# Performance work log

Hardware: AMD Instinct MI355X
Metric: run time of the kernel (lower is better)

The kernel has to match this reference:

```python
import jax, jax.numpy as jnp
import numpy as np

B, S, D, H = 2, 2048, 1024, 16
DH = D // H


def setup_inputs() -> dict:
    key = jax.random.key(0)
    ks = jax.random.split(key, 6)
    scale = 0.02
    X = jax.random.normal(ks[0], (B, S, D), dtype=jnp.float32)
    masks = jax.random.randint(ks[1], (B, S), 0, 2).astype(jnp.int32)
    Wq = jax.random.normal(ks[2], (D, D), dtype=jnp.float32) * scale
    Wk = jax.random.normal(ks[3], (D, D), dtype=jnp.float32) * scale
    Wv = jax.random.normal(ks[4], (D, D), dtype=jnp.float32) * scale
    Wo = jax.random.normal(ks[5], (D, D), dtype=jnp.float32) * scale
    return {"X": X, "masks": masks, "Wq": Wq, "Wk": Wk, "Wv": Wv, "Wo": Wo}


def reference(X, masks, Wq, Wk, Wv, Wo):
    b, s, d = X.shape
    masks_b = masks.astype(bool)                       # [B,S] key validity
    lookahead = jnp.triu(jnp.ones((s, s), dtype=bool), 1)  # [S,S] future positions
    pad = ~masks_b[:, None, :]                         # [B,1,S] -> invalid keys
    invalid = pad | lookahead[None, :, :]              # [B,S,S]
    valid = (~invalid)[:, None, :, :].astype(X.dtype)  # [B,1,S,S]

    def split_heads(Y):  # [B,S,D] -> [B,H,S,DH]
        return Y.reshape(b, s, H, DH).transpose(0, 2, 1, 3)

    Q = split_heads(X @ Wq.T)
    K = split_heads(X @ Wk.T)
    V = split_heads(X @ Wv.T)

    Qn = Q / jnp.sqrt(jnp.sum(Q * Q, axis=-1, keepdims=True))
    Kn = K / jnp.sqrt(jnp.sum(K * K, axis=-1, keepdims=True))

    scores = jnp.einsum('bhqd,bhkd->bhqk', Qn, Kn)     # cosine similarities
    att = jax.nn.relu(scores) * valid                  # relu + causal/pad mask
    ctx = jnp.einsum('bhqk,bhkd->bhqd', att, V)
    ctx = ctx * masks_b[:, None, :, None].astype(X.dtype)  # zero padded queries

    out = ctx.transpose(0, 2, 1, 3).reshape(b, s, d)
    return out @ Wo.T
```

## Files before the change

### kernel.cpp

```cpp
#include <hip/hip_runtime.h>
#include <hip/hip_bf16.h>

#define BB 2
#define SS 2048
#define DD 1024
#define HH 16
#define MMR (BB*SS)
#define ND3 3072

typedef __hip_bfloat16 bf;
typedef __bf16 bf16x8 __attribute__((ext_vector_type(8)));
typedef float f32x4 __attribute__((ext_vector_type(4)));
typedef float f32x16 __attribute__((ext_vector_type(16)));

#define VMCNT(n) asm volatile("s_waitcnt vmcnt(" #n ")" ::: "memory")

__device__ __forceinline__ f32x4 mfma16(bf16x8 a, bf16x8 b, f32x4 c) {
    return __builtin_amdgcn_mfma_f32_16x16x32_bf16(a, b, c, 0, 0, 0);
}
__device__ __forceinline__ f32x16 mfma32(bf16x8 a, bf16x8 b, f32x16 c) {
    return __builtin_amdgcn_mfma_f32_32x32x16_bf16(a, b, c, 0, 0, 0);
}
__device__ __forceinline__ unsigned cvt_pk_bf16(float lo, float hi) {
    unsigned r;
    asm("v_cvt_pk_bf16_f32 %0, %1, %2" : "=v"(r) : "v"(lo), "v"(hi));
    return r;
}
__device__ __forceinline__ void pl32swap(unsigned& a, unsigned& b) {
    asm("v_permlane32_swap_b32 %0, %1" : "+v"(a), "+v"(b));
}
__device__ __forceinline__ void glds16(const bf* g, bf* l) {
    __builtin_amdgcn_global_load_lds(
        (const __attribute__((address_space(1))) void*)g,
        (__attribute__((address_space(3))) void*)l,
        16, 0, 0);
}

__global__ __launch_bounds__(256) void k_convert(const float* __restrict__ X,
                                                 const float* __restrict__ Wq,
                                                 const float* __restrict__ Wk,
                                                 const float* __restrict__ Wv,
                                                 const float* __restrict__ Wo,
                                                 bf* __restrict__ Xb,
                                                 bf* __restrict__ Wqkv,
                                                 bf* __restrict__ Wob) {
    const int bid = blockIdx.x;
    const float* src;
    bf* dst;
    int off;
    if (bid < 4096) {
        src = X; dst = Xb; off = bid;
    } else {
        const int r = (bid - 4096) >> 10;
        src = (r == 0) ? Wq : (r == 1) ? Wk : (r == 2) ? Wv : Wo;
        dst = (r < 3) ? (Wqkv + (size_t)r * 1048576) : Wob;
        off = (bid - 4096) & 1023;
    }
    const int j = (off * 256 + threadIdx.x) * 4;
    float4 v = *(const float4*)(src + j);
    bf tmp[4];
    tmp[0] = __float2bfloat16(v.x);
    tmp[1] = __float2bfloat16(v.y);
    tmp[2] = __float2bfloat16(v.z);
    tmp[3] = __float2bfloat16(v.w);
    *(uint2*)(dst + j) = *(const uint2*)tmp;
}

__global__ __launch_bounds__(512, 6) void k_gemm8(const bf* __restrict__ A,
                                                  const bf* __restrict__ Bt,
                                                  const int* __restrict__ masks,
                                                  bf* __restrict__ Qn,
                                                  bf* __restrict__ Kn,
                                                  bf* __restrict__ Vt,
                                                  int nx) {
    constexpr int K = 1024;
    constexpr int T = K >> 5;
    __shared__ __align__(16) bf Asm[3][128 * 32];
    __shared__ __align__(16) bf Bsm[3][128 * 32];
    const int tid = threadIdx.x;
    const int w = tid >> 6, lane = tid & 63, g = lane >> 4, rl = lane & 15;
    const int cpx = gridDim.x >> 3;
    const int swz = (blockIdx.x & 7) * cpx + (blockIdx.x >> 3);
    const int m0 = (swz / nx) * 128, n0 = (swz % nx) * 128;
    const int wr = (w >> 1) * 32, wc = (w & 1) * 64;
    const int lrow = lane >> 2, lseg = lane & 3;
    const int xseg = lseg ^ ((lrow >> 1) & 3);

    f32x4 acc[2][4] = {};

    const bf* asr = A + (size_t)(m0 + w * 16 + lrow) * K + xseg * 8;
    const bf* bsr = Bt + (size_t)(n0 + w * 16 + lrow) * K + xseg * 8;
    bf* const adst = &Asm[0][w * 512];
    bf* const bdst = &Bsm[0][w * 512];

    auto stageP = [&](int buf) {
        glds16(asr, adst + buf * 4096);
        glds16(bsr, bdst + buf * 4096);
        asr += 32; bsr += 32;
    };

    auto computeT = [&](const bf* Ab, const bf* Bb) {
        bf16x8 af[2], bfr[4];
#pragma unroll
        for (int m = 0; m < 2; ++m) {
            const int row = wr + m * 16 + rl;
            af[m] = __builtin_bit_cast(bf16x8,
                *(const int4*)&Ab[row * 32 + (g ^ ((row >> 1) & 3)) * 8]);
        }
#pragma unroll
        for (int n = 0; n < 4; ++n) {
            const int row = wc + n * 16 + rl;
            bfr[n] = __builtin_bit_cast(bf16x8,
                *(const int4*)&Bb[row * 32 + (g ^ ((row >> 1) & 3)) * 8]);
        }
        __builtin_amdgcn_s_setprio(1);
#pragma unroll
        for (int m = 0; m < 2; ++m)
#pragma unroll
            for (int n = 0; n < 4; ++n)
                acc[m][n] = mfma16(af[m], bfr[n], acc[m][n]);
        __builtin_amdgcn_s_setprio(0);
    };

    auto step = [&](auto CURc, auto NXTc, int t) {
        constexpr int CUR = decltype(CURc)::value;
        constexpr int NXT = decltype(NXTc)::value;
        __builtin_amdgcn_sched_barrier(0);
        if (t < T - 1) { VMCNT(2); } else { VMCNT(0); }
        __builtin_amdgcn_s_barrier();
        __builtin_amdgcn_sched_barrier(0);
        if (t + 2 < T) stageP(NXT);
        computeT(&Asm[CUR][0], &Bsm[CUR][0]);
    };
    using c0 = std::integral_constant<int, 0>;
    using c1 = std::integral_constant<int, 1>;
    using c2 = std::integral_constant<int, 2>;

    stageP(0);
    stageP(1);
#pragma unroll 1
    for (int t = 0; t < 30; t += 3) {
        step(c0{}, c2{}, t);
        step(c1{}, c0{}, t + 1);
        step(c2{}, c1{}, t + 2);
    }
    step(c0{}, c2{}, 30);
    step(c1{}, c0{}, 31);

    const int ncol0 = n0 + wc;
    if (ncol0 < 2048) {
        bf* dst = (ncol0 < 1024) ? Qn : Kn;
        const int h2 = (ncol0 >> 6) & 15;
#pragma unroll
        for (int m = 0; m < 2; ++m) {
#pragma unroll
            for (int ri = 0; ri < 4; ++ri) {
                const int row = m0 + wr + m * 16 + g * 4 + ri;
                float ss = 0.f;
#pragma unroll
                for (int n = 0; n < 4; ++n) ss += acc[m][n][ri] * acc[m][n][ri];
#pragma unroll
                for (int d = 1; d < 16; d <<= 1) ss += __shfl_xor(ss, d, 64);
                const float sc = rsqrtf(ss) * (masks[row] ? 1.0f : 0.0f);
                const int b = row >> 11, s = row & 2047;
                const size_t base = ((size_t)(b * HH + h2) * SS + s) * 64;
#pragma unroll
                for (int n = 0; n < 4; ++n)
                    dst[base + n * 16 + rl] = __float2bfloat16(acc[m][n][ri] * sc);
            }
        }
    } else {
        const int h2 = (ncol0 - 2048) >> 6;
        const int b = (m0 + wr) >> 11;
        const int sb = ((m0 + wr) & 2047) + g * 4;
#pragma unroll
        for (int m = 0; m < 2; ++m)
#pragma unroll
            for (int n = 0; n < 4; ++n) {
                const int d = n * 16 + rl;
                bf t4[4];
#pragma unroll
                for (int ri = 0; ri < 4; ++ri) t4[ri] = __float2bfloat16(acc[m][n][ri]);
                *(uint2*)&Vt[((size_t)(b * HH + h2) * 64 + d) * SS + sb + m * 16] =
                    *(uint2*)t4;
            }
    }
}

__global__ __launch_bounds__(256) void k_gemm(const bf* __restrict__ A,
                                              const bf* __restrict__ Bt,
                                              float* __restrict__ Cf,
                                              int nx, int N, int K) {
    constexpr int BM = 64, BN = 128;
    __shared__ __align__(16) bf Asm[3][BM * 32];
    __shared__ __align__(16) bf Bsm[3][BN * 32];
    const int tid = threadIdx.x;
    const int w = tid >> 6, lane = tid & 63, g = lane >> 4, rl = lane & 15;
    const int cpx = gridDim.x >> 3;
    const int swz = (blockIdx.x & 7) * cpx + (blockIdx.x >> 3);
    const int m0 = (swz / nx) * BM, n0 = (swz % nx) * BN;
    const int wr = (w >> 1) * 32, wc = (w & 1) * 64;
    const int lrow = lane >> 2, lseg = lane & 3;
    const int xseg = lseg ^ ((lrow >> 1) & 3);

    f32x4 acc[2][4] = {};
    const bf* Ap = A + (size_t)m0 * K;
    const bf* Bp = Bt + (size_t)n0 * K;

    auto stage = [&](int bi, int k0) {
        glds16(Ap + (size_t)(w * 16 + lrow) * K + k0 + xseg * 8, &Asm[bi][w * 512]);
#pragma unroll
        for (int u = 0; u < 2; ++u)
            glds16(Bp + (size_t)(u * 64 + w * 16 + lrow) * K + k0 + xseg * 8,
                   &Bsm[bi][(u * 64 + w * 16) * 32]);
    };

    const int T = K >> 5;
    stage(0, 0);
    stage(1, 32);
    int cur = 0, nxt = 2;
    for (int t = 0; t < T; ++t) {
        __builtin_amdgcn_sched_barrier(0);
        if (t < T - 1) { VMCNT(3); } else { VMCNT(0); }
        __builtin_amdgcn_s_barrier();
        __builtin_amdgcn_sched_barrier(0);
        if (t + 2 < T) stage(nxt, (t + 2) * 32);

        const bf* Ab = Asm[cur];
        const bf* Bb = Bsm[cur];
        bf16x8 af[2], bfr[4];
#pragma unroll
        for (int m = 0; m < 2; ++m) {
            const int row = wr + m * 16 + rl;
            af[m] = __builtin_bit_cast(bf16x8,
                *(const int4*)&Ab[row * 32 + (g ^ ((row >> 1) & 3)) * 8]);
        }
#pragma unroll
        for (int n = 0; n < 4; ++n) {
            const int row = wc + n * 16 + rl;
            bfr[n] = __builtin_bit_cast(bf16x8,
                *(const int4*)&Bb[row * 32 + (g ^ ((row >> 1) & 3)) * 8]);
        }
        __builtin_amdgcn_s_setprio(1);
#pragma unroll
        for (int m = 0; m < 2; ++m)
#pragma unroll
            for (int n = 0; n < 4; ++n)
                acc[m][n] = mfma16(af[m], bfr[n], acc[m][n]);
        __builtin_amdgcn_s_setprio(0);

        cur = (cur == 2) ? 0 : cur + 1;
        nxt = (nxt == 2) ? 0 : nxt + 1;
    }

#pragma unroll
    for (int m = 0; m < 2; ++m)
#pragma unroll
        for (int n = 0; n < 4; ++n)
#pragma unroll
            for (int ri = 0; ri < 4; ++ri)
                Cf[(size_t)(m0 + wr + m * 16 + g * 4 + ri) * N + n0 + wc + n * 16 + rl] =
                    acc[m][n][ri];
}

__global__ __launch_bounds__(256) void k_attn(const bf* __restrict__ Qn,
                                              const bf* __restrict__ Kn,
                                              const bf* __restrict__ Vt,
                                              bf* __restrict__ Ctx) {
    __shared__ __align__(16) bf Ksm[2][64 * 64];
    __shared__ __align__(16) bf Vsm[2][64 * 64];

    const int idx = blockIdx.x;
    const int qt = 31 - (idx >> 5);
    const int by = idx & 31;
    const int b = by >> 4, h = by & 15;
    const int tid = threadIdx.x;
    const int w = tid >> 6, lane = tid & 63;
    const int l31 = lane & 31, hl = lane >> 5;
    const int qh = w >> 1;
    const int kp = w & 1;
    const int qw = qt * 64 + qh * 32;
    const int qg = qw + l31;

    const bf* Qp = Qn + (size_t)by * SS * 64;
    const bf* Kp = Kn + (size_t)by * SS * 64;
    const bf* Vp = Vt + (size_t)by * 64 * SS;

    bf16x8 aqs[4];
#pragma unroll
    for (int st = 0; st < 4; ++st)
        aqs[st] = __builtin_bit_cast(bf16x8,
            *(const int4*)(Qp + (size_t)(qw + l31) * 64 + st * 16 + hl * 8));

    const int srow = lane >> 3;
    const int sblk = (lane & 7) ^ srow;

    const bf* ksr = Kp + (size_t)(w * 16 + srow) * 64 + sblk * 8;
    const bf* vsr = Vp + (size_t)(w * 16 + srow) * SS + sblk * 8;
    bf* const kdst = &Ksm[0][w * 1024];
    bf* const vdst = &Vsm[0][w * 1024];

    auto stageP = [&](int buf, const bf* ks, const bf* vs) {
        glds16(ks,            kdst + buf * 4096);
        glds16(ks + 512,      kdst + buf * 4096 + 512);
        glds16(vs,            vdst + buf * 4096);
        glds16(vs + 8 * SS,   vdst + buf * 4096 + 512);
    };

    f32x16 accd[2] = {};

    auto doTile = [&](const bf* Ks, const bf* Vs, int t) {
        const int kb = t * 64 + kp * 32;
        if (kb > qw + 31) return;
        f32x16 pc = {};
        const int r = kp * 32 + l31;
#pragma unroll
        for (int st = 0; st < 4; ++st) {
            bf16x8 ak = __builtin_bit_cast(bf16x8,
                *(const int4*)&Ks[r * 64 + (((2 * st + hl) ^ (r & 7)) << 3)]);
            pc = mfma32(ak, aqs[st], pc);
        }
        const bool dg = (kb + 31 > qw);
        float pv[16];
#pragma unroll
        for (int m2 = 0; m2 < 16; ++m2) {
            float v = fmaxf(pc[m2], 0.0f);
            if (dg) {
                const int kg = kb + (m2 & 3) + 8 * (m2 >> 2) + 4 * hl;
                if (kg > qg) v = 0.0f;
            }
            pv[m2] = v;
        }
        unsigned P[8];
#pragma unroll
        for (int m2 = 0; m2 < 8; ++m2) P[m2] = cvt_pk_bf16(pv[2 * m2], pv[2 * m2 + 1]);
        pl32swap(P[0], P[2]);
        pl32swap(P[1], P[3]);
        pl32swap(P[4], P[6]);
        pl32swap(P[5], P[7]);
#pragma unroll
        for (int s = 0; s < 2; ++s) {
            uint4 pw = {P[4 * s + 0], P[4 * s + 1], P[4 * s + 2], P[4 * s + 3]};
            bf16x8 pa = __builtin_bit_cast(bf16x8, pw);
#pragma unroll
            for (int dt = 0; dt < 2; ++dt) {
                const int d = dt * 32 + l31;
                const int slot = kp * 4 + s * 2 + hl;
                bf16x8 bv = __builtin_bit_cast(bf16x8,
                    *(const int4*)&Vs[d * 64 + ((slot ^ (d & 7)) << 3)]);
                accd[dt] = mfma32(pa, bv, accd[dt]);
            }
        }
    };

    stageP(0, ksr, vsr);
    ksr += 4096; vsr += 64;
    __syncthreads();

    int t = 0;
    while (t + 1 <= qt) {
        stageP(1, ksr, vsr);
        ksr += 4096; vsr += 64;
        doTile(&Ksm[0][0], &Vsm[0][0], t);
        __syncthreads();
        if (t + 2 <= qt) {
            stageP(0, ksr, vsr);
            ksr += 4096; vsr += 64;
        }
        doTile(&Ksm[1][0], &Vsm[1][0], t + 1);
        __syncthreads();
        t += 2;
    }
    if (t <= qt) {
        doTile(&Ksm[0][0], &Vsm[0][0], t);
        __syncthreads();
    }

    float* red = (float*)&Ksm[0][0];
    if (kp == 1) {
#pragma unroll
        for (int dt = 0; dt < 2; ++dt)
#pragma unroll
            for (int m2 = 0; m2 < 16; ++m2)
                red[qh * 2048 + (dt * 16 + m2) * 64 + lane] = accd[dt][m2];
    }
    __syncthreads();
    if (kp == 0) {
#pragma unroll
        for (int dt = 0; dt < 2; ++dt)
#pragma unroll
            for (int m2 = 0; m2 < 16; ++m2) {
                const float v = accd[dt][m2] + red[qh * 2048 + (dt * 16 + m2) * 64 + lane];
                const int q = qw + (m2 & 3) + 8 * (m2 >> 2) + 4 * hl;
                const int d = dt * 32 + l31;
                Ctx[(size_t)(b * SS + q) * DD + h * 64 + d] = __float2bfloat16(v);
            }
    }
}

extern "C" void kernel_launch(void* const* d_in, const int* in_sizes, int n_in,
                              void* d_out, int out_size, void* d_ws, size_t ws_size,
                              hipStream_t stream) {
    const float* X  = (const float*)d_in[0];
    const int* masks = (const int*)d_in[1];
    const float* Wq = (const float*)d_in[2];
    const float* Wk = (const float*)d_in[3];
    const float* Wv = (const float*)d_in[4];
    const float* Wo = (const float*)d_in[5];
    float* out = (float*)d_out;
    char* ws = (char*)d_ws;

    const size_t MB = 1024 * 1024;
    bf* Xb   = (bf*)(ws);
    bf* Wqkv = (bf*)(ws + 8  * MB);
    bf* Wob  = (bf*)(ws + 14 * MB);
    bf* Qn   = (bf*)(ws + 16 * MB);
    bf* Kn   = (bf*)(ws + 24 * MB);
    bf* Vt   = (bf*)(ws + 32 * MB);
    bf* Ctx  = (bf*)(ws + 40 * MB);

    k_convert<<<8192, 256, 0, stream>>>(X, Wq, Wk, Wv, Wo, Xb, Wqkv, Wob);

    k_gemm8<<<(ND3 / 128) * (MMR / 128), 512, 0, stream>>>(
        Xb, Wqkv, masks, Qn, Kn, Vt, ND3 / 128);

    k_attn<<<1024, 256, 0, stream>>>(Qn, Kn, Vt, Ctx);

    k_gemm<<<(DD / 128) * (MMR / 64), 256, 0, stream>>>(
        Ctx, Wob, out, DD / 128, DD, DD);
}
```

Baseline: 94.86 us.

## Enlarge attention query tile to 128 rows with 512-thread blocks

```diff
diff --git a/kernel.cpp b/kernel.cpp
--- a/kernel.cpp
+++ b/kernel.cpp
@@ -263,15 +263,16 @@
                     acc[m][n][ri];
 }
 
-__global__ __launch_bounds__(256) void k_attn(const bf* __restrict__ Qn,
+__global__ __launch_bounds__(512) void k_attn(const bf* __restrict__ Qn,
                                               const bf* __restrict__ Kn,
                                               const bf* __restrict__ Vt,
                                               bf* __restrict__ Ctx) {
-    __shared__ __align__(16) bf Ksm[2][64 * 64];
-    __shared__ __align__(16) bf Vsm[2][64 * 64];
+    __shared__ __align__(16) bf smem[16384];
+    bf* const Ksm0 = smem;
+    bf* const Vsm0 = smem + 8192;
 
     const int idx = blockIdx.x;
-    const int qt = 31 - (idx >> 5);
+    const int qt = 15 - (idx >> 5);
     const int by = idx & 31;
     const int b = by >> 4, h = by & 15;
     const int tid = threadIdx.x;
@@ -279,7 +280,7 @@
     const int l31 = lane & 31, hl = lane >> 5;
     const int qh = w >> 1;
     const int kp = w & 1;
-    const int qw = qt * 64 + qh * 32;
+    const int qw = qt * 128 + qh * 32;
     const int qg = qw + l31;
 
     const bf* Qp = Qn + (size_t)by * SS * 64;
@@ -295,16 +296,15 @@
     const int srow = lane >> 3;
     const int sblk = (lane & 7) ^ srow;
 
-    const bf* ksr = Kp + (size_t)(w * 16 + srow) * 64 + sblk * 8;
-    const bf* vsr = Vp + (size_t)(w * 16 + srow) * SS + sblk * 8;
-    bf* const kdst = &Ksm[0][w * 1024];
-    bf* const vdst = &Vsm[0][w * 1024];
-
-    auto stageP = [&](int buf, const bf* ks, const bf* vs) {
-        glds16(ks,            kdst + buf * 4096);
-        glds16(ks + 512,      kdst + buf * 4096 + 512);
-        glds16(vs,            vdst + buf * 4096);
-        glds16(vs + 8 * SS,   vdst + buf * 4096 + 512);
+    const bf* ksr = Kp + (size_t)(w * 8 + srow) * 64 + sblk * 8;
+    const bf* vsr = Vp + (size_t)(w * 8 + srow) * SS + sblk * 8;
+    bf* const kdst = Ksm0 + w * 512;
+    bf* const vdst = Vsm0 + w * 512;
+
+    auto stageP = [&](int buf) {
+        glds16(ksr, kdst + buf * 4096);
+        glds16(vsr, vdst + buf * 4096);
+        ksr += 4096; vsr += 64;
     };
 
     f32x16 accd[2] = {};
@@ -353,30 +353,22 @@
         }
     };
 
-    stageP(0, ksr, vsr);
-    ksr += 4096; vsr += 64;
+    stageP(0);
     __syncthreads();
 
+    const int nt = 2 * qt + 2;
     int t = 0;
-    while (t + 1 <= qt) {
-        stageP(1, ksr, vsr);
-        ksr += 4096; vsr += 64;
-        doTile(&Ksm[0][0], &Vsm[0][0], t);
+    while (t + 1 < nt) {
+        stageP(1);
+        doTile(Ksm0, Vsm0, t);
         __syncthreads();
-        if (t + 2 <= qt) {
-            stageP(0, ksr, vsr);
-            ksr += 4096; vsr += 64;
-        }
-        doTile(&Ksm[1][0], &Vsm[1][0], t + 1);
+        if (t + 2 < nt) stageP(0);
+        doTile(Ksm0 + 4096, Vsm0 + 4096, t + 1);
         __syncthreads();
         t += 2;
     }
-    if (t <= qt) {
-        doTile(&Ksm[0][0], &Vsm[0][0], t);
-        __syncthreads();
-    }
-
-    float* red = (float*)&Ksm[0][0];
+
+    float* red = (float*)smem;
     if (kp == 1) {
 #pragma unroll
         for (int dt = 0; dt < 2; ++dt)
@@ -424,7 +416,7 @@
     k_gemm8<<<(ND3 / 128) * (MMR / 128), 512, 0, stream>>>(
         Xb, Wqkv, masks, Qn, Kn, Vt, ND3 / 128);
 
-    k_attn<<<1024, 256, 0, stream>>>(Qn, Kn, Vt, Ctx);
+    k_attn<<<512, 512, 0, stream>>>(Qn, Kn, Vt, Ctx);
 
     k_gemm<<<(DD / 128) * (MMR / 64), 256, 0, stream>>>(
         Ctx, Wob, out, DD / 128, DD, DD);
```

Result: no change. 94.36 us (-0.5%).
